# Kernel tuning notes

Hardware: AMD Instinct MI355X
Metric: run time of the kernel (lower is better)

## Reference

```python
import jax, jax.numpy as jnp
import numpy as np

N, TI, ENC_DIM, DEC_DIM, ATT_DIM = 32, 2000, 512, 512, 512


def setup_inputs() -> dict:
    key = jax.random.key(0)
    ks = jax.random.split(key, 8)
    enc_pad = jax.random.normal(ks[0], (N, TI, ENC_DIM), dtype=jnp.float32)
    dec_prev = jax.random.normal(ks[1], (N, DEC_DIM), dtype=jnp.float32)
    ali_prev = jax.random.uniform(ks[2], (N, TI), dtype=jnp.float32)
    # lengths in [Ti//2, Ti], force one full-length row (module uses max(enc_len) as mask width)
    enc_len = jax.random.randint(ks[3], (N,), TI // 2, TI + 1)
    enc_len = enc_len.at[0].set(TI)
    # learned params (nn.Linear layout: W [out, in])
    s_e = 1.0 / np.sqrt(ENC_DIM)
    s_d = 1.0 / np.sqrt(DEC_DIM)
    s_a = 1.0 / np.sqrt(ATT_DIM)
    W_enc = jax.random.uniform(ks[4], (ATT_DIM, ENC_DIM), minval=-s_e, maxval=s_e, dtype=jnp.float32)
    b_enc = jax.random.uniform(ks[5], (ATT_DIM,), minval=-s_e, maxval=s_e, dtype=jnp.float32)
    W_dec = jax.random.uniform(ks[6], (ATT_DIM, DEC_DIM), minval=-s_d, maxval=s_d, dtype=jnp.float32)
    w_v = jax.random.uniform(ks[7], (ATT_DIM,), minval=-s_a, maxval=s_a, dtype=jnp.float32)
    return {"enc_pad": enc_pad, "enc_len": enc_len, "dec_prev": dec_prev,
            "ali_prev": ali_prev, "W_enc": W_enc, "b_enc": b_enc,
            "W_dec": W_dec, "w_v": w_v}


def reference(enc_pad, enc_len, dec_prev, ali_prev, W_enc, b_enc, W_dec, w_v):
    # enc_part: N x Ti x A  (enc_proj with bias)
    enc_part = jnp.einsum('ntd,ad->nta', enc_pad, W_enc) + b_enc
    # dec_part: N x A  (dec_proj, no bias)
    dec_part = jnp.einsum('nd,ad->na', dec_prev, W_dec)
    # additive score e = w^T tanh(enc_part + dec_part): N x Ti
    e = jnp.einsum('nta,a->nt', jnp.tanh(enc_part + dec_part[:, None, :]), w_v)
    # padding mask: positions >= enc_len are masked
    mask = jnp.arange(e.shape[1]) >= enc_len[:, None]  # N x Ti
    e = jnp.where(mask, -jnp.inf, e)
    ali = jax.nn.softmax(e, axis=1)  # N x Ti
    ctx = jnp.einsum('nt,ntd->nd', ali, enc_pad)  # N x D_enc
    return (ali, ctx)
```

## Files before the change

### kernel.cpp

```cpp
#include <hip/hip_runtime.h>
#include <stdint.h>


#define NB  32
#define TI  2000
#define ED  512
#define AD  512
#define M_TOT (NB * TI)
#define NSPLIT 20
#define TCHUNK (TI / NSPLIT)
#define MT  500
#define KT  8
#define TILE_BYTES  16384
#define TILE_HALVES 8192

using f16x8 = __attribute__((ext_vector_type(8))) _Float16;
using f32x4 = __attribute__((ext_vector_type(4))) float;

__device__ __forceinline__ int swz(int r, int c2) { return (r * 128 + c2) ^ ((r & 7) << 4); }

#define GLD16(g, l)                                                     \
    __builtin_amdgcn_global_load_lds(                                   \
        (const __attribute__((address_space(1))) void*)(g),             \
        (__attribute__((address_space(3))) void*)(l), 16, 0, 0)

__device__ __forceinline__ float fast_tanh(float s) {
    s = fminf(fmaxf(s, -15.f), 15.f);
    float t = __expf(2.f * s);
    return __fdividef(t - 1.f, t + 1.f);
}

__global__ void k_convert(const float* __restrict__ enc, const float* __restrict__ Wenc,
                          _Float16* __restrict__ X16, _Float16* __restrict__ W16) {
    int bx = blockIdx.x;
    const float* src;
    char* dstb;
    if (bx < MT * KT) {
        int mt = bx >> 3, kt = bx & 7;
        src  = enc + (size_t)mt * 128 * ED + kt * 64;
        dstb = (char*)(X16 + (size_t)bx * TILE_HALVES);
    } else {
        int wt = bx - MT * KT;
        int at = wt >> 3, kt = wt & 7;
        src  = Wenc + (size_t)at * 128 * ED + kt * 64;
        dstb = (char*)(W16 + (size_t)wt * TILE_HALVES);
    }
    int tid = threadIdx.x;
#pragma unroll
    for (int i = 0; i < 4; ++i) {
        int o  = i * 4096 + tid * 16;
        int r  = o >> 7;
        int c2 = o & 127;
        const float* s = src + (size_t)r * ED + (c2 >> 1);
        float4 a = *(const float4*)s;
        float4 b = *(const float4*)(s + 4);
        f16x8 h;
        h[0] = (_Float16)a.x; h[1] = (_Float16)a.y; h[2] = (_Float16)a.z; h[3] = (_Float16)a.w;
        h[4] = (_Float16)b.x; h[5] = (_Float16)b.y; h[6] = (_Float16)b.z; h[7] = (_Float16)b.w;
        *(f16x8*)(dstb + swz(r, c2)) = h;
    }
}

__global__ void k_decdb(const float* __restrict__ dec_prev,
                        const float* __restrict__ W_dec,
                        const float* __restrict__ b_enc,
                        float* __restrict__ db) {
    int n = blockIdx.x;
    __shared__ float xd[ED];
    for (int k = threadIdx.x; k < ED; k += 256) xd[k] = dec_prev[n * ED + k];
    __syncthreads();
    for (int a = threadIdx.x; a < AD; a += 256) {
        const float* wr = W_dec + (size_t)a * ED;
        float s = 0.f;
#pragma unroll 8
        for (int k = 0; k < ED; k += 4) {
            float4 w = *(const float4*)(wr + k);
            s += xd[k] * w.x + xd[k + 1] * w.y + xd[k + 2] * w.z + xd[k + 3] * w.w;
        }
        db[n * AD + a] = s + b_enc[a];
    }
}

__launch_bounds__(256, 4)
__global__ void k_score(const _Float16* __restrict__ X16, const _Float16* __restrict__ W16,
                        const float* __restrict__ db, const float* __restrict__ wv,
                        float* __restrict__ e_part) {
    __shared__ alignas(16) char Xs[TILE_BYTES];
    __shared__ alignas(16) char Ws[TILE_BYTES];
    __shared__ float e_red[2][128];

    int fid = blockIdx.x;
    int g = fid >> 5, rr = fid & 31;
    int at = rr >> 3, l = rr & 7;
    int mt = g * 8 + l;
    if (mt >= MT) return;

    const int tid  = threadIdx.x;
    const int lane = tid & 63;
    const int w    = tid >> 6;
    const int wr   = w >> 1;
    const int wc   = w & 1;
    const int m0   = mt * 128;
    const int a0   = at * 128;

    const char* xbase = (const char*)(X16 + (size_t)(mt * KT) * TILE_HALVES);
    const char* wbase = (const char*)(W16 + (size_t)(at * KT) * TILE_HALVES);

    f32x4 acc[4][4];
#pragma unroll
    for (int rb = 0; rb < 4; ++rb)
#pragma unroll
        for (int cb = 0; cb < 4; ++cb) acc[rb][cb] = (f32x4){0.f, 0.f, 0.f, 0.f};

    const int lr   = lane & 15;
    const int lk2  = ((lane >> 4) << 3) * 2;
    const int xorv = (lr & 7) << 4;
    const int stoff = w * 1024 + lane * 16;

    for (int kt = 0; kt < KT; ++kt) {
        const char* xs = xbase + kt * TILE_BYTES + stoff;
        const char* ws = wbase + kt * TILE_BYTES + stoff;
#pragma unroll
        for (int i = 0; i < 4; ++i) {
            GLD16(xs + i * 4096, Xs + i * 4096 + w * 1024);
            GLD16(ws + i * 4096, Ws + i * 4096 + w * 1024);
        }
        __syncthreads();

#pragma unroll
        for (int kb = 0; kb < 2; ++kb) {
            f16x8 aF[4], bF[4];
#pragma unroll
            for (int rb = 0; rb < 4; ++rb) {
                int r = wr * 64 + rb * 16 + lr;
                aF[rb] = *(const f16x8*)(Xs + ((r * 128 + kb * 64 + lk2) ^ xorv));
            }
#pragma unroll
            for (int cb = 0; cb < 4; ++cb) {
                int r = wc * 64 + cb * 16 + lr;
                bF[cb] = *(const f16x8*)(Ws + ((r * 128 + kb * 64 + lk2) ^ xorv));
            }
#pragma unroll
            for (int rb = 0; rb < 4; ++rb)
#pragma unroll
                for (int cb = 0; cb < 4; ++cb)
                    acc[rb][cb] = __builtin_amdgcn_mfma_f32_16x16x32_f16(
                        aF[rb], bF[cb], acc[rb][cb], 0, 0, 0);
        }
        __syncthreads();
    }

    const int lg = lane >> 4;
    float wvv[4];
#pragma unroll
    for (int cb = 0; cb < 4; ++cb) wvv[cb] = wv[a0 + wc * 64 + cb * 16 + lr];

#pragma unroll
    for (int rb = 0; rb < 4; ++rb) {
#pragma unroll
        for (int i = 0; i < 4; ++i) {
            int row_local = wr * 64 + rb * 16 + lg * 4 + i;
            int m = m0 + row_local;
            int n = m / TI;
            const float* dbp = db + (size_t)n * AD + a0 + wc * 64;
            float rs = 0.f;
#pragma unroll
            for (int cb = 0; cb < 4; ++cb) {
                float s = acc[rb][cb][i] + dbp[cb * 16 + lr];
                rs += fast_tanh(s) * wvv[cb];
            }
            rs += __shfl_xor(rs, 1);
            rs += __shfl_xor(rs, 2);
            rs += __shfl_xor(rs, 4);
            rs += __shfl_xor(rs, 8);
            if (lr == 0) e_red[wc][row_local] = rs;
        }
    }
    __syncthreads();
    if (tid < 128)
        e_part[(size_t)at * M_TOT + m0 + tid] = e_red[0][tid] + e_red[1][tid];
}

__launch_bounds__(256, 2)
__global__ void k_score_fb(const float* __restrict__ X, const float* __restrict__ W,
                           const float* __restrict__ db, const float* __restrict__ wv,
                           float* __restrict__ e_part) {
    __shared__ alignas(16) _Float16 Xs[128][72];
    __shared__ alignas(16) _Float16 Ws[128][72];
    __shared__ float e_red[2][128];

    const int tid = threadIdx.x, lane = tid & 63, wid = tid >> 6;
    const int wr = wid >> 1, wc = wid & 1;
    const int m0 = blockIdx.x * 128, a0 = blockIdx.y * 128;

    f32x4 acc[4][4];
#pragma unroll
    for (int rb = 0; rb < 4; ++rb)
#pragma unroll
        for (int cb = 0; cb < 4; ++cb) acc[rb][cb] = (f32x4){0.f, 0.f, 0.f, 0.f};

    const int lr = lane & 15;
    const int lk = (lane >> 4) << 3;

    for (int kt = 0; kt < ED; kt += 64) {
#pragma unroll
        for (int i = 0; i < 4; ++i) {
            int idx = tid + i * 256, r = idx >> 3, c = (idx & 7) << 3;
            const float* gx = X + (size_t)(m0 + r) * ED + kt + c;
            float4 x0 = *(const float4*)gx, x1 = *(const float4*)(gx + 4);
            f16x8 hx;
            hx[0] = (_Float16)x0.x; hx[1] = (_Float16)x0.y; hx[2] = (_Float16)x0.z; hx[3] = (_Float16)x0.w;
            hx[4] = (_Float16)x1.x; hx[5] = (_Float16)x1.y; hx[6] = (_Float16)x1.z; hx[7] = (_Float16)x1.w;
            *(f16x8*)&Xs[r][c] = hx;
            const float* gw = W + (size_t)(a0 + r) * ED + kt + c;
            float4 w0 = *(const float4*)gw, w1 = *(const float4*)(gw + 4);
            f16x8 hw;
            hw[0] = (_Float16)w0.x; hw[1] = (_Float16)w0.y; hw[2] = (_Float16)w0.z; hw[3] = (_Float16)w0.w;
            hw[4] = (_Float16)w1.x; hw[5] = (_Float16)w1.y; hw[6] = (_Float16)w1.z; hw[7] = (_Float16)w1.w;
            *(f16x8*)&Ws[r][c] = hw;
        }
        __syncthreads();
#pragma unroll
        for (int kb = 0; kb < 64; kb += 32) {
            f16x8 aF[4], bF[4];
#pragma unroll
            for (int rb = 0; rb < 4; ++rb) aF[rb] = *(const f16x8*)&Xs[wr * 64 + rb * 16 + lr][kb + lk];
#pragma unroll
            for (int cb = 0; cb < 4; ++cb) bF[cb] = *(const f16x8*)&Ws[wc * 64 + cb * 16 + lr][kb + lk];
#pragma unroll
            for (int rb = 0; rb < 4; ++rb)
#pragma unroll
                for (int cb = 0; cb < 4; ++cb)
                    acc[rb][cb] = __builtin_amdgcn_mfma_f32_16x16x32_f16(aF[rb], bF[cb], acc[rb][cb], 0, 0, 0);
        }
        __syncthreads();
    }

    const int lg = lane >> 4;
    float wvv[4];
#pragma unroll
    for (int cb = 0; cb < 4; ++cb) wvv[cb] = wv[a0 + wc * 64 + cb * 16 + lr];
#pragma unroll
    for (int rb = 0; rb < 4; ++rb) {
#pragma unroll
        for (int i = 0; i < 4; ++i) {
            int row_local = wr * 64 + rb * 16 + lg * 4 + i;
            int m = m0 + row_local;
            int n = m / TI;
            const float* dbp = db + (size_t)n * AD + a0 + wc * 64;
            float rs = 0.f;
#pragma unroll
            for (int cb = 0; cb < 4; ++cb) {
                float s = acc[rb][cb][i] + dbp[cb * 16 + lr];
                rs += fast_tanh(s) * wvv[cb];
            }
            rs += __shfl_xor(rs, 1);
            rs += __shfl_xor(rs, 2);
            rs += __shfl_xor(rs, 4);
            rs += __shfl_xor(rs, 8);
            if (lr == 0) e_red[wc][row_local] = rs;
        }
    }
    __syncthreads();
    if (tid < 128)
        e_part[(size_t)blockIdx.y * M_TOT + m0 + tid] = e_red[0][tid] + e_red[1][tid];
}

__global__ void k_softmax(const float* __restrict__ e_part,
                          const int* __restrict__ enc_len,
                          float* __restrict__ ali) {
    int n = blockIdx.x;
    int len = enc_len[n];
    __shared__ float se[TI];
    __shared__ float redm[4];
    __shared__ float reds[4];
    int tid = threadIdx.x;
    int lane = tid & 63, wid = tid >> 6;

    for (int t = tid; t < TI; t += 256) {
        se[t] = e_part[n * TI + t] + e_part[M_TOT + n * TI + t] +
                e_part[2 * M_TOT + n * TI + t] + e_part[3 * M_TOT + n * TI + t];
    }
    __syncthreads();

    float mx = -1e30f;
    for (int t = tid; t < len; t += 256) mx = fmaxf(mx, se[t]);
#pragma unroll
    for (int o = 32; o >= 1; o >>= 1) mx = fmaxf(mx, __shfl_xor(mx, o));
    if (lane == 0) redm[wid] = mx;
    __syncthreads();
    mx = fmaxf(fmaxf(redm[0], redm[1]), fmaxf(redm[2], redm[3]));

    float sm = 0.f;
    for (int t = tid; t < len; t += 256) {
        float ex = __expf(se[t] - mx);
        se[t] = ex;
        sm += ex;
    }
#pragma unroll
    for (int o = 32; o >= 1; o >>= 1) sm += __shfl_xor(sm, o);
    if (lane == 0) reds[wid] = sm;
    __syncthreads();
    float inv = 1.f / (reds[0] + reds[1] + reds[2] + reds[3]);

    for (int t = tid; t < TI; t += 256)
        ali[n * TI + t] = (t < len) ? se[t] * inv : 0.f;
}

__global__ void k_ctxpart16(const _Float16* __restrict__ X16, const float* __restrict__ ali,
                            float* __restrict__ cpart) {
    int s = blockIdx.x, n = blockIdx.y;
    int tid = threadIdx.x;
    int sub = tid >> 6;
    int dc  = (tid & 63) * 8;
    int ktile = dc >> 6;
    int c2 = (dc & 63) * 2;
    float acc[8] = {0.f, 0.f, 0.f, 0.f, 0.f, 0.f, 0.f, 0.f};
    for (int t = s * TCHUNK + sub; t < (s + 1) * TCHUNK; t += 4) {
        int m = n * TI + t;
        int mt2 = m >> 7, r = m & 127;
        const char* p = (const char*)(X16 + (size_t)(mt2 * KT + ktile) * TILE_HALVES);
        f16x8 v = *(const f16x8*)(p + swz(r, c2));
        float a = ali[m];
#pragma unroll
        for (int j = 0; j < 8; ++j) acc[j] = fmaf(a, (float)v[j], acc[j]);
    }
    __shared__ float red[4][ED];
#pragma unroll
    for (int j = 0; j < 8; ++j) red[sub][dc + j] = acc[j];
    __syncthreads();
    if (sub == 0) {
#pragma unroll
        for (int j = 0; j < 8; ++j) {
            float sm = red[0][dc + j] + red[1][dc + j] + red[2][dc + j] + red[3][dc + j];
            cpart[((size_t)(n * NSPLIT + s)) * ED + dc + j] = sm;
        }
    }
}

__global__ void k_ctxpart(const float* __restrict__ enc,
                          const float* __restrict__ ali,
                          float* __restrict__ cpart) {
    int s = blockIdx.x;
    int n = blockIdx.y;
    int d0 = threadIdx.x * 2;
    const float* base = enc + ((size_t)n * TI + s * TCHUNK) * ED + d0;
    const float* ap = ali + n * TI + s * TCHUNK;
    float ax = 0.f, ay = 0.f;
#pragma unroll 4
    for (int t = 0; t < TCHUNK; ++t) {
        float a = ap[t];
        float2 v = *(const float2*)(base + (size_t)t * ED);
        ax = fmaf(a, v.x, ax);
        ay = fmaf(a, v.y, ay);
    }
    float2 r; r.x = ax; r.y = ay;
    *(float2*)&cpart[((size_t)(n * NSPLIT + s)) * ED + d0] = r;
}

__global__ void k_ctxred(const float* __restrict__ cpart, float* __restrict__ ctx) {
    int n = blockIdx.x;
    for (int d = threadIdx.x; d < ED; d += 256) {
        float sum = 0.f;
#pragma unroll
        for (int s = 0; s < NSPLIT; ++s) sum += cpart[((size_t)(n * NSPLIT + s)) * ED + d];
        ctx[(size_t)n * ED + d] = sum;
    }
}

extern "C" void kernel_launch(void* const* d_in, const int* in_sizes, int n_in,
                              void* d_out, int out_size, void* d_ws, size_t ws_size,
                              hipStream_t stream) {
    const float* enc_pad  = (const float*)d_in[0];
    const int*   enc_len  = (const int*)d_in[1];
    const float* dec_prev = (const float*)d_in[2];
    const float* W_enc    = (const float*)d_in[4];
    const float* b_enc    = (const float*)d_in[5];
    const float* W_dec    = (const float*)d_in[6];
    const float* w_v      = (const float*)d_in[7];

    float* out = (float*)d_out;
    float* ali = out;
    float* ctx = out + M_TOT;

    float* ws     = (float*)d_ws;
    float* db     = ws;
    float* e_part = ws + NB * AD;
    float* cpart  = e_part + 4 * M_TOT;
    size_t fp_floats = (size_t)NB * AD + 4 * M_TOT + (size_t)NB * NSPLIT * ED;
    _Float16* X16 = (_Float16*)((char*)d_ws + fp_floats * 4);
    _Float16* W16 = X16 + (size_t)MT * KT * TILE_HALVES;
    size_t need = fp_floats * 4 + ((size_t)MT * KT + 32) * TILE_BYTES;
    bool big = ws_size >= need;

    hipLaunchKernelGGL(k_decdb, dim3(NB), dim3(256), 0, stream, dec_prev, W_dec, b_enc, db);
    if (big) {
        hipLaunchKernelGGL(k_convert, dim3(MT * KT + 32), dim3(256), 0, stream,
                           enc_pad, W_enc, X16, W16);
        hipLaunchKernelGGL(k_score, dim3(2016), dim3(256), 0, stream,
                           X16, W16, db, w_v, e_part);
    } else {
        hipLaunchKernelGGL(k_score_fb, dim3(MT, 4), dim3(256), 0, stream,
                           enc_pad, W_enc, db, w_v, e_part);
    }
    hipLaunchKernelGGL(k_softmax, dim3(NB), dim3(256), 0, stream, e_part, enc_len, ali);
    if (big) {
        hipLaunchKernelGGL(k_ctxpart16, dim3(NSPLIT, NB), dim3(256), 0, stream, X16, ali, cpart);
    } else {
        hipLaunchKernelGGL(k_ctxpart, dim3(NSPLIT, NB), dim3(256), 0, stream, enc_pad, ali, cpart);
    }
    hipLaunchKernelGGL(k_ctxred, dim3(NB), dim3(256), 0, stream, cpart, ctx);
}
```

Before: 147.0 us.

## Use 256x256 double-buffered score GEMM tiles and fuse dec projection into convert

Replaces the 128x128 score GEMM with a 512-thread kernel computing 256x256 tiles. It double-buffers LDS staging so global-to-LDS loads overlap MFMA work, and raises wave priority around the MFMA block. The decoder projection is folded into the conversion kernel as extra blocks, removing one launch, and softmax now sums two partial-score planes instead of four. The larger tiles reuse each loaded tile more, at the cost of 128KB of LDS and more accumulator registers per thread, which may limit occupancy.

After: 138.9 us. 5.5% less time.

```diff
diff --git a/kernel.cpp b/kernel.cpp
--- a/kernel.cpp
+++ b/kernel.cpp
@@ -10,6 +10,7 @@
 #define NSPLIT 20
 #define TCHUNK (TI / NSPLIT)
 #define MT  500
+#define MT2 250
 #define KT  8
 #define TILE_BYTES  16384
 #define TILE_HALVES 8192
@@ -17,7 +18,7 @@
 using f16x8 = __attribute__((ext_vector_type(8))) _Float16;
 using f32x4 = __attribute__((ext_vector_type(4))) float;
 
-__device__ __forceinline__ int swz(int r, int c2) { return (r * 128 + c2) ^ ((r & 7) << 4); }
+__device__ __forceinline__ int swz(int r, int c) { return (r * 128 + c) ^ ((r & 7) << 4); }
 
 #define GLD16(g, l)                                                     \
     __builtin_amdgcn_global_load_lds(                                   \
@@ -31,8 +32,28 @@
 }
 
 __global__ void k_convert(const float* __restrict__ enc, const float* __restrict__ Wenc,
-                          _Float16* __restrict__ X16, _Float16* __restrict__ W16) {
+                          _Float16* __restrict__ X16, _Float16* __restrict__ W16,
+                          const float* __restrict__ dec_prev, const float* __restrict__ W_dec,
+                          const float* __restrict__ b_enc, float* __restrict__ db) {
+    __shared__ float xd[ED];
     int bx = blockIdx.x;
+    int tid = threadIdx.x;
+    if (bx >= MT * KT + 32) {
+        int n = bx - (MT * KT + 32);
+        for (int k = tid; k < ED; k += 256) xd[k] = dec_prev[n * ED + k];
+        __syncthreads();
+        for (int a = tid; a < AD; a += 256) {
+            const float* wr = W_dec + (size_t)a * ED;
+            float s = 0.f;
+#pragma unroll 8
+            for (int k = 0; k < ED; k += 4) {
+                float4 w = *(const float4*)(wr + k);
+                s += xd[k] * w.x + xd[k + 1] * w.y + xd[k + 2] * w.z + xd[k + 3] * w.w;
+            }
+            db[n * AD + a] = s + b_enc[a];
+        }
+        return;
+    }
     const float* src;
     char* dstb;
     if (bx < MT * KT) {
@@ -45,7 +66,6 @@
         src  = Wenc + (size_t)at * 128 * ED + kt * 64;
         dstb = (char*)(W16 + (size_t)wt * TILE_HALVES);
     }
-    int tid = threadIdx.x;
 #pragma unroll
     for (int i = 0; i < 4; ++i) {
         int o  = i * 4096 + tid * 16;
@@ -81,88 +101,106 @@
     }
 }
 
-__launch_bounds__(256, 4)
-__global__ void k_score(const _Float16* __restrict__ X16, const _Float16* __restrict__ W16,
-                        const float* __restrict__ db, const float* __restrict__ wv,
-                        float* __restrict__ e_part) {
-    __shared__ alignas(16) char Xs[TILE_BYTES];
-    __shared__ alignas(16) char Ws[TILE_BYTES];
-    __shared__ float e_red[2][128];
+__device__ __forceinline__ void stage_tiles(const char* xb, const char* wb,
+                                            char* dA, char* dB, int kt, int o) {
+    const char* xs = xb + kt * TILE_BYTES + o;
+    const char* ws = wb + kt * TILE_BYTES + o;
+    GLD16(xs,                           dA + o);
+    GLD16(xs + 8192,                    dA + o + 8192);
+    GLD16(xs + KT * TILE_BYTES,         dA + o + 16384);
+    GLD16(xs + KT * TILE_BYTES + 8192,  dA + o + 24576);
+    GLD16(ws,                           dB + o);
+    GLD16(ws + 8192,                    dB + o + 8192);
+    GLD16(ws + KT * TILE_BYTES,         dB + o + 16384);
+    GLD16(ws + KT * TILE_BYTES + 8192,  dB + o + 24576);
+}
+
+__launch_bounds__(512, 2)
+__global__ void k_score256(const _Float16* __restrict__ X16, const _Float16* __restrict__ W16,
+                           const float* __restrict__ db, const float* __restrict__ wv,
+                           float* __restrict__ e_part) {
+    __shared__ alignas(16) char As0[32768];
+    __shared__ alignas(16) char As1[32768];
+    __shared__ alignas(16) char Bs0[32768];
+    __shared__ alignas(16) char Bs1[32768];
 
     int fid = blockIdx.x;
-    int g = fid >> 5, rr = fid & 31;
-    int at = rr >> 3, l = rr & 7;
-    int mt = g * 8 + l;
-    if (mt >= MT) return;
+    int g = fid >> 4, r = fid & 15;
+    int at2 = r >> 3;
+    int mt2 = g * 8 + (r & 7);
+    if (mt2 >= MT2) return;
 
     const int tid  = threadIdx.x;
     const int lane = tid & 63;
     const int w    = tid >> 6;
-    const int wr   = w >> 1;
-    const int wc   = w & 1;
-    const int m0   = mt * 128;
-    const int a0   = at * 128;
-
-    const char* xbase = (const char*)(X16 + (size_t)(mt * KT) * TILE_HALVES);
-    const char* wbase = (const char*)(W16 + (size_t)(at * KT) * TILE_HALVES);
-
-    f32x4 acc[4][4];
-#pragma unroll
-    for (int rb = 0; rb < 4; ++rb)
+    const int wm   = w >> 2;
+    const int wn   = w & 3;
+    const int m0   = mt2 * 256;
+    const int a0   = at2 * 256;
+
+    const char* xb = (const char*)X16 + (size_t)(mt2 * 2 * KT) * TILE_BYTES;
+    const char* wb = (const char*)W16 + (size_t)(at2 * 2 * KT) * TILE_BYTES;
+
+    const int lr    = lane & 15;
+    const int lk2   = (lane >> 4) * 16;
+    const int wmoff = wm * 16384;
+    const int wnoff = (wn >> 1) * 16384;
+    const int wnrow = (wn & 1) * 64;
+    const int o     = tid * 16;
+
+    f32x4 acc[8][4];
+#pragma unroll
+    for (int rb = 0; rb < 8; ++rb)
 #pragma unroll
         for (int cb = 0; cb < 4; ++cb) acc[rb][cb] = (f32x4){0.f, 0.f, 0.f, 0.f};
 
-    const int lr   = lane & 15;
-    const int lk2  = ((lane >> 4) << 3) * 2;
-    const int xorv = (lr & 7) << 4;
-    const int stoff = w * 1024 + lane * 16;
-
-    for (int kt = 0; kt < KT; ++kt) {
-        const char* xs = xbase + kt * TILE_BYTES + stoff;
-        const char* ws = wbase + kt * TILE_BYTES + stoff;
-#pragma unroll
-        for (int i = 0; i < 4; ++i) {
-            GLD16(xs + i * 4096, Xs + i * 4096 + w * 1024);
-            GLD16(ws + i * 4096, Ws + i * 4096 + w * 1024);
-        }
-        __syncthreads();
-
-#pragma unroll
-        for (int kb = 0; kb < 2; ++kb) {
-            f16x8 aF[4], bF[4];
-#pragma unroll
-            for (int rb = 0; rb < 4; ++rb) {
-                int r = wr * 64 + rb * 16 + lr;
-                aF[rb] = *(const f16x8*)(Xs + ((r * 128 + kb * 64 + lk2) ^ xorv));
-            }
-#pragma unroll
-            for (int cb = 0; cb < 4; ++cb) {
-                int r = wc * 64 + cb * 16 + lr;
-                bF[cb] = *(const f16x8*)(Ws + ((r * 128 + kb * 64 + lk2) ^ xorv));
-            }
-#pragma unroll
-            for (int rb = 0; rb < 4; ++rb)
-#pragma unroll
-                for (int cb = 0; cb < 4; ++cb)
-                    acc[rb][cb] = __builtin_amdgcn_mfma_f32_16x16x32_f16(
-                        aF[rb], bF[cb], acc[rb][cb], 0, 0, 0);
-        }
-        __syncthreads();
-    }
-
+#define COMPUTE(sA, sB)                                                          \
+    {                                                                            \
+        _Pragma("unroll")                                                        \
+        for (int kb = 0; kb < 2; ++kb) {                                         \
+            f16x8 aF[8], bF[4];                                                  \
+            _Pragma("unroll")                                                    \
+            for (int rb = 0; rb < 8; ++rb)                                       \
+                aF[rb] = *(const f16x8*)((sA) + wmoff + swz(rb * 16 + lr, kb * 64 + lk2)); \
+            _Pragma("unroll")                                                    \
+            for (int cb = 0; cb < 4; ++cb)                                       \
+                bF[cb] = *(const f16x8*)((sB) + wnoff + swz(wnrow + cb * 16 + lr, kb * 64 + lk2)); \
+            __builtin_amdgcn_s_setprio(1);                                       \
+            _Pragma("unroll")                                                    \
+            for (int rb = 0; rb < 8; ++rb)                                       \
+                _Pragma("unroll")                                                \
+                for (int cb = 0; cb < 4; ++cb)                                   \
+                    acc[rb][cb] = __builtin_amdgcn_mfma_f32_16x16x32_f16(        \
+                        aF[rb], bF[cb], acc[rb][cb], 0, 0, 0);                   \
+            __builtin_amdgcn_s_setprio(0);                                       \
+        }                                                                        \
+    }
+
+    stage_tiles(xb, wb, As0, Bs0, 0, o); __syncthreads();
+    stage_tiles(xb, wb, As1, Bs1, 1, o); COMPUTE(As0, Bs0); __syncthreads();
+    stage_tiles(xb, wb, As0, Bs0, 2, o); COMPUTE(As1, Bs1); __syncthreads();
+    stage_tiles(xb, wb, As1, Bs1, 3, o); COMPUTE(As0, Bs0); __syncthreads();
+    stage_tiles(xb, wb, As0, Bs0, 4, o); COMPUTE(As1, Bs1); __syncthreads();
+    stage_tiles(xb, wb, As1, Bs1, 5, o); COMPUTE(As0, Bs0); __syncthreads();
+    stage_tiles(xb, wb, As0, Bs0, 6, o); COMPUTE(As1, Bs1); __syncthreads();
+    stage_tiles(xb, wb, As1, Bs1, 7, o); COMPUTE(As0, Bs0); __syncthreads();
+    COMPUTE(As1, Bs1); __syncthreads();
+#undef COMPUTE
+
+    float* e_red = (float*)As0;
     const int lg = lane >> 4;
     float wvv[4];
 #pragma unroll
-    for (int cb = 0; cb < 4; ++cb) wvv[cb] = wv[a0 + wc * 64 + cb * 16 + lr];
-
-#pragma unroll
-    for (int rb = 0; rb < 4; ++rb) {
+    for (int cb = 0; cb < 4; ++cb) wvv[cb] = wv[a0 + wn * 64 + cb * 16 + lr];
+
+#pragma unroll
+    for (int rb = 0; rb < 8; ++rb) {
 #pragma unroll
         for (int i = 0; i < 4; ++i) {
-            int row_local = wr * 64 + rb * 16 + lg * 4 + i;
+            int row_local = wm * 128 + rb * 16 + lg * 4 + i;
             int m = m0 + row_local;
             int n = m / TI;
-            const float* dbp = db + (size_t)n * AD + a0 + wc * 64;
+            const float* dbp = db + (size_t)n * AD + a0 + wn * 64;
             float rs = 0.f;
 #pragma unroll
             for (int cb = 0; cb < 4; ++cb) {
@@ -173,12 +211,13 @@
             rs += __shfl_xor(rs, 2);
             rs += __shfl_xor(rs, 4);
             rs += __shfl_xor(rs, 8);
-            if (lr == 0) e_red[wc][row_local] = rs;
-        }
-    }
-    __syncthreads();
-    if (tid < 128)
-        e_part[(size_t)at * M_TOT + m0 + tid] = e_red[0][tid] + e_red[1][tid];
+            if (lr == 0) e_red[wn * 256 + row_local] = rs;
+        }
+    }
+    __syncthreads();
+    if (tid < 256)
+        e_part[(size_t)at2 * M_TOT + m0 + tid] =
+            e_red[tid] + e_red[256 + tid] + e_red[512 + tid] + e_red[768 + tid];
 }
 
 __launch_bounds__(256, 2)
@@ -268,7 +307,7 @@
 
 __global__ void k_softmax(const float* __restrict__ e_part,
                           const int* __restrict__ enc_len,
-                          float* __restrict__ ali) {
+                          float* __restrict__ ali, int nparts) {
     int n = blockIdx.x;
     int len = enc_len[n];
     __shared__ float se[TI];
@@ -278,8 +317,9 @@
     int lane = tid & 63, wid = tid >> 6;
 
     for (int t = tid; t < TI; t += 256) {
-        se[t] = e_part[n * TI + t] + e_part[M_TOT + n * TI + t] +
-                e_part[2 * M_TOT + n * TI + t] + e_part[3 * M_TOT + n * TI + t];
+        float s = 0.f;
+        for (int p = 0; p < nparts; ++p) s += e_part[(size_t)p * M_TOT + n * TI + t];
+        se[t] = s;
     }
     __syncthreads();
 
@@ -393,20 +433,18 @@
     size_t need = fp_floats * 4 + ((size_t)MT * KT + 32) * TILE_BYTES;
     bool big = ws_size >= need;
 
-    hipLaunchKernelGGL(k_decdb, dim3(NB), dim3(256), 0, stream, dec_prev, W_dec, b_enc, db);
     if (big) {
-        hipLaunchKernelGGL(k_convert, dim3(MT * KT + 32), dim3(256), 0, stream,
-                           enc_pad, W_enc, X16, W16);
-        hipLaunchKernelGGL(k_score, dim3(2016), dim3(256), 0, stream,
+        hipLaunchKernelGGL(k_convert, dim3(MT * KT + 64), dim3(256), 0, stream,
+                           enc_pad, W_enc, X16, W16, dec_prev, W_dec, b_enc, db);
+        hipLaunchKernelGGL(k_score256, dim3(512), dim3(512), 0, stream,
                            X16, W16, db, w_v, e_part);
+        hipLaunchKernelGGL(k_softmax, dim3(NB), dim3(256), 0, stream, e_part, enc_len, ali, 2);
+        hipLaunchKernelGGL(k_ctxpart16, dim3(NSPLIT, NB), dim3(256), 0, stream, X16, ali, cpart);
     } else {
+        hipLaunchKernelGGL(k_decdb, dim3(NB), dim3(256), 0, stream, dec_prev, W_dec, b_enc, db);
         hipLaunchKernelGGL(k_score_fb, dim3(MT, 4), dim3(256), 0, stream,
                            enc_pad, W_enc, db, w_v, e_part);
-    }
-    hipLaunchKernelGGL(k_softmax, dim3(NB), dim3(256), 0, stream, e_part, enc_len, ali);
-    if (big) {
-        hipLaunchKernelGGL(k_ctxpart16, dim3(NSPLIT, NB), dim3(256), 0, stream, X16, ali, cpart);
-    } else {
+        hipLaunchKernelGGL(k_softmax, dim3(NB), dim3(256), 0, stream, e_part, enc_len, ali, 4);
         hipLaunchKernelGGL(k_ctxpart, dim3(NSPLIT, NB), dim3(256), 0, stream, enc_pad, ali, cpart);
     }
     hipLaunchKernelGGL(k_ctxred, dim3(NB), dim3(256), 0, stream, cpart, ctx);
```
